# Kernel tuning notes

Measured on AMD Instinct MI355X. Metric: run time of the kernel, lower is better.

Reference implementation:

```python
import jax, jax.numpy as jnp
import numpy as np

D_IN, D_OUT, K = 128, 128, 64
X_MIN, X_MAX = 0.0, 1.0
EPS = 1e-12


def _pchip_slopes(y, x):
    # y: [..., K], x: [K] strictly increasing -> slopes [..., K]. Assumes K >= 3.
    h = x[1:] - x[:-1]                      # [K-1]
    delta = (y[..., 1:] - y[..., :-1]) / (h + EPS)
    h0, h1 = h[:-1], h[1:]
    w1 = 2.0 * h1 + h0
    w2 = h1 + 2.0 * h0
    d0_, d1_ = delta[..., :-1], delta[..., 1:]
    same_sign = d0_ * d1_ > 0
    denom = w1 / (d0_ + EPS) + w2 / (d1_ + EPS)
    d_int = jnp.where(same_sign, (w1 + w2) / (denom + EPS), 0.0)  # [..., K-2]
    d_first = ((2.0 * h[0] + h[1]) * delta[..., 0] - h[0] * delta[..., 1]) / (h[0] + h[1] + EPS)
    d_last = ((2.0 * h[-1] + h[-2]) * delta[..., -1] - h[-1] * delta[..., -2]) / (h[-1] + h[-2] + EPS)

    def limit(di, de):
        di = jnp.where(di * de <= 0, 0.0, di)
        return jnp.where(jnp.abs(di) > 3.0 * jnp.abs(de), 3.0 * de, di)

    d_first = limit(d_first, delta[..., 0])
    d_last = limit(d_last, delta[..., -1])
    return jnp.concatenate([d_first[..., None], d_int, d_last[..., None]], axis=-1)


def setup_inputs() -> dict:
    key = jax.random.key(0)
    k1, k2 = jax.random.split(key)
    x = jax.random.normal(k1, (4096, D_IN), dtype=jnp.float32)
    coeffs = 0.2 * jax.random.normal(k2, (D_OUT, D_IN, K), dtype=jnp.float32)
    bias = jnp.zeros((D_OUT,), dtype=jnp.float32)
    knots = jnp.linspace(X_MIN, X_MAX, K, dtype=jnp.float32)
    return {"x": x, "coeffs": coeffs, "bias": bias, "knots": knots}


def reference(x, coeffs, bias, knots):
    B = x.shape[0]
    slopes = _pchip_slopes(coeffs, knots)              # [d_out, d_in, K]
    h = (X_MAX - X_MIN) / (K - 1)

    xc = jnp.clip(x, X_MIN, X_MAX)                     # [B, d_in]
    idx = jnp.clip(jnp.floor((xc - X_MIN) / h).astype(jnp.int32), 0, K - 2)
    t = (xc - (X_MIN + idx.astype(x.dtype) * h)) / h   # [B, d_in]
    t2 = t * t
    t3 = t2 * t
    h00 = 2 * t3 - 3 * t2 + 1
    h10 = t3 - 2 * t2 + t
    h01 = -2 * t3 + 3 * t2
    h11 = t3 - t2

    ct = jnp.transpose(coeffs, (1, 2, 0))              # [d_in, K, d_out]
    dt = jnp.transpose(slopes, (1, 2, 0))              # [d_in, K, d_out]
    ii = jnp.arange(D_IN)[None, :]                     # [1, d_in]
    y0 = ct[ii, idx]                                   # [B, d_in, d_out]
    y1 = ct[ii, idx + 1]
    d0 = dt[ii, idx]
    d1 = dt[ii, idx + 1]

    yi = (h00[..., None] * y0 + h10[..., None] * h * d0
          + h01[..., None] * y1 + h11[..., None] * h * d1)  # [B, d_in, d_out]

    # linear extrapolation beyond the knot range
    y_left = ct[:, 0, :][None] + dt[:, 0, :][None] * (x - X_MIN)[..., None]
    y_right = ct[:, -1, :][None] + dt[:, -1, :][None] * (x - X_MAX)[..., None]
    yi = jnp.where((x < X_MIN)[..., None], y_left, yi)
    yi = jnp.where((x > X_MAX)[..., None], y_right, yi)

    return yi.sum(axis=1) + bias[None, :]              # [B, d_out]
```

## Files before the change

kernel.cpp:

```cpp
#include <hip/hip_runtime.h>

#define KN 64
#define DIN 128
#define DOUT 128
#define EPSF 1e-12f
#define HF (1.0f / 63.0f)

typedef _Float16 h2 __attribute__((ext_vector_type(2)));

#if defined(__has_builtin)
#if __has_builtin(__builtin_amdgcn_fdot2)
#define FDOT2(a, b, c) __builtin_amdgcn_fdot2((a), (b), (c), false)
#endif
#endif
#ifndef FDOT2
static __device__ __forceinline__ float FDOT2(h2 a, h2 b, float c) {
    return c + (float)a.x * (float)b.x + (float)a.y * (float)b.y;
}
#endif


__global__ __launch_bounds__(256) void kan_precompute(
    const float* __restrict__ coeffs,
    const float* __restrict__ knots,
    unsigned int* __restrict__ tb)
{
    const int i      = blockIdx.x >> 1;
    const int o_base = (blockIdx.x & 1) << 6;
    const int wave   = threadIdx.x >> 6;
    const int lane   = threadIdx.x & 63;

    __shared__ float ys[64][65];
    __shared__ float ds[64][65];

    float kn  = knots[lane];
    float kn1 = (lane < 63) ? knots[lane + 1] : 0.0f;
    float hk  = kn1 - kn;
    float hm1 = __shfl_up(hk, 1);
    float h1v = __shfl_down(hk, 1);
    float hm2 = __shfl_up(hk, 2);

    for (int ol = wave; ol < 64; ol += 4) {
        const int o = o_base + ol;
        float y = coeffs[(o * DIN + i) * KN + lane];
        float ynext = __shfl_down(y, 1);
        float delta = (lane < 63) ? (ynext - y) / (hk + EPSF) : 0.0f;
        float dm1 = __shfl_up(delta, 1);

        float w1v = 2.0f * hk + hm1;
        float w2v = hk + 2.0f * hm1;
        float denom = w1v / (dm1 + EPSF) + w2v / (delta + EPSF);
        float d = (dm1 * delta > 0.0f) ? (w1v + w2v) / (denom + EPSF) : 0.0f;

        float d1v = __shfl_down(delta, 1);
        if (lane == 0) {
            float df = ((2.0f * hk + h1v) * delta - hk * d1v) / (hk + h1v + EPSF);
            if (df * delta <= 0.0f) df = 0.0f;
            else if (fabsf(df) > 3.0f * fabsf(delta)) df = 3.0f * delta;
            d = df;
        }
        float dm2 = __shfl_up(delta, 2);
        if (lane == 63) {
            float dl = ((2.0f * hm1 + hm2) * dm1 - hm1 * dm2) / (hm1 + hm2 + EPSF);
            if (dl * dm1 <= 0.0f) dl = 0.0f;
            else if (fabsf(dl) > 3.0f * fabsf(dm1)) dl = 3.0f * dm1;
            d = dl;
        }
        ys[ol][lane] = y;
        ds[ol][lane] = d * HF;
    }
    __syncthreads();

    const int ol = threadIdx.x & 63;
    const int kb = threadIdx.x >> 6;
    for (int k = kb; k < KN; k += 4) {
        h2 v;
        v.x = (_Float16)ys[ol][k];
        v.y = (_Float16)ds[ol][k];
        tb[(i * KN + k) * DOUT + o_base + ol] = __builtin_bit_cast(unsigned int, v);
    }
}

__global__ __launch_bounds__(256) void kan_main(
    const float* __restrict__ x,
    const uint2* __restrict__ tb2,
    const float* __restrict__ bias,
    float* __restrict__ out)
{
    const int b0   = blockIdx.x << 2;
    const int tid  = threadIdx.x;
    const int wv   = tid >> 6;
    const int lane = tid & 63;

    __shared__ uint4 wl[4][DIN];

    #pragma unroll
    for (int p = tid; p < 4 * DIN; p += 256) {
        const int bl = p >> 7;
        const int i  = p & 127;
        float xv = x[(b0 + bl) * DIN + i];
        float xc = fminf(fmaxf(xv, 0.0f), 1.0f);
        int idx = (int)floorf(xc * 63.0f);
        idx = idx < 0 ? 0 : (idx > 62 ? 62 : idx);
        float t = xc * 63.0f - (float)idx;
        float t2 = t * t, t3 = t2 * t;
        float w0 = 2.0f * t3 - 3.0f * t2 + 1.0f;
        float w1 = t3 - 2.0f * t2 + t;
        float w2 = 3.0f * t2 - 2.0f * t3;
        float w3 = t3 - t2;
        if (xv < 0.0f)      { w0 = 1.0f; w1 = xv * 63.0f; w2 = 0.0f; w3 = 0.0f; idx = 0; }
        else if (xv > 1.0f) { w0 = 0.0f; w1 = 0.0f; w2 = 1.0f; w3 = (xv - 1.0f) * 63.0f; idx = 62; }
        h2 w01; w01.x = (_Float16)w0; w01.y = (_Float16)w1;
        h2 w23; w23.x = (_Float16)w2; w23.y = (_Float16)w3;
        uint4 q;
        q.x = __builtin_bit_cast(unsigned int, w01);
        q.y = __builtin_bit_cast(unsigned int, w23);
        q.z = (unsigned int)idx;
        q.w = 0u;
        wl[bl][i] = q;
    }
    __syncthreads();

    float acc0 = 0.0f, acc1 = 0.0f;
    #pragma unroll 8
    for (int i = 0; i < DIN; ++i) {
        uint4 q = wl[wv][i];
        h2 w01 = __builtin_bit_cast(h2, q.x);
        h2 w23 = __builtin_bit_cast(h2, q.y);
        int base = ((i << 6) + (int)q.z) * 64 + lane;
        uint2 A = tb2[base];
        uint2 B = tb2[base + 64];
        acc0 = FDOT2(w01, __builtin_bit_cast(h2, A.x), acc0);
        acc0 = FDOT2(w23, __builtin_bit_cast(h2, B.x), acc0);
        acc1 = FDOT2(w01, __builtin_bit_cast(h2, A.y), acc1);
        acc1 = FDOT2(w23, __builtin_bit_cast(h2, B.y), acc1);
    }

    const int o0 = lane << 1;
    float2 bo = *reinterpret_cast<const float2*>(&bias[o0]);
    float2 r; r.x = acc0 + bo.x; r.y = acc1 + bo.y;
    *reinterpret_cast<float2*>(&out[(b0 + wv) * DOUT + o0]) = r;
}

extern "C" void kernel_launch(void* const* d_in, const int* in_sizes, int n_in,
                              void* d_out, int out_size, void* d_ws, size_t ws_size,
                              hipStream_t stream) {
    const float* x      = (const float*)d_in[0];
    const float* coeffs = (const float*)d_in[1];
    const float* bias   = (const float*)d_in[2];
    const float* knots  = (const float*)d_in[3];
    float* out = (float*)d_out;
    unsigned int* tb = (unsigned int*)d_ws;

    kan_precompute<<<256, 256, 0, stream>>>(coeffs, knots, tb);
    kan_main<<<1024, 256, 0, stream>>>(x, (const uint2*)tb, bias, out);
}
```

Baseline: 107.5 us.

## Store adjacent-knot pairs in table and split d_in across waves

The precompute table now stores, for each (input, segment, output), the fp16 value/slope pair for both knot k and knot k+1 together. The main kernel can then fetch all four operands with a single 16-byte load per lane instead of two 8-byte loads from separate rows. The main kernel also splits the 128 inputs across two waves per batch row and combines the partial sums through shared memory, doubling the grid to 2048 blocks. This adds a synchronisation, doubles the table's footprint, and spreads the precompute over more, smaller blocks.

```diff
diff --git a/kernel.cpp b/kernel.cpp
--- a/kernel.cpp
+++ b/kernel.cpp
@@ -23,15 +23,15 @@
 __global__ __launch_bounds__(256) void kan_precompute(
     const float* __restrict__ coeffs,
     const float* __restrict__ knots,
-    unsigned int* __restrict__ tb)
+    uint2* __restrict__ tb)
 {
-    const int i      = blockIdx.x >> 1;
-    const int o_base = (blockIdx.x & 1) << 6;
+    const int i      = blockIdx.x >> 2;
+    const int o_base = (blockIdx.x & 3) << 5;
     const int wave   = threadIdx.x >> 6;
     const int lane   = threadIdx.x & 63;
 
-    __shared__ float ys[64][65];
-    __shared__ float ds[64][65];
+    __shared__ float ys[32][65];
+    __shared__ float ds[32][65];
 
     float kn  = knots[lane];
     float kn1 = (lane < 63) ? knots[lane + 1] : 0.0f;
@@ -40,8 +40,10 @@
     float h1v = __shfl_down(hk, 1);
     float hm2 = __shfl_up(hk, 2);
 
-    for (int ol = wave; ol < 64; ol += 4) {
-        const int o = o_base + ol;
+    #pragma unroll
+    for (int m = 0; m < 8; ++m) {
+        const int ol = wave + (m << 2);
+        const int o  = o_base + ol;
         float y = coeffs[(o * DIN + i) * KN + lane];
         float ynext = __shfl_down(y, 1);
         float delta = (lane < 63) ? (ynext - y) / (hk + EPSF) : 0.0f;
@@ -71,34 +73,42 @@
     }
     __syncthreads();
 
-    const int ol = threadIdx.x & 63;
-    const int kb = threadIdx.x >> 6;
-    for (int k = kb; k < KN; k += 4) {
-        h2 v;
-        v.x = (_Float16)ys[ol][k];
-        v.y = (_Float16)ds[ol][k];
-        tb[(i * KN + k) * DOUT + o_base + ol] = __builtin_bit_cast(unsigned int, v);
+    const int ol2 = threadIdx.x & 31;
+    const int j0  = threadIdx.x >> 5;
+    #pragma unroll
+    for (int m = 0; m < 8; ++m) {
+        const int j = j0 + (m << 3);
+        if (j < 63) {
+            h2 lo; lo.x = (_Float16)ys[ol2][j];     lo.y = (_Float16)ds[ol2][j];
+            h2 hi; hi.x = (_Float16)ys[ol2][j + 1]; hi.y = (_Float16)ds[ol2][j + 1];
+            uint2 v;
+            v.x = __builtin_bit_cast(unsigned int, lo);
+            v.y = __builtin_bit_cast(unsigned int, hi);
+            tb[((i << 6) + j) * DOUT + o_base + ol2] = v;
+        }
     }
 }
 
 __global__ __launch_bounds__(256) void kan_main(
     const float* __restrict__ x,
-    const uint2* __restrict__ tb2,
+    const uint4* __restrict__ tb4,
     const float* __restrict__ bias,
     float* __restrict__ out)
 {
-    const int b0   = blockIdx.x << 2;
+    const int b0   = blockIdx.x << 1;
     const int tid  = threadIdx.x;
     const int wv   = tid >> 6;
+    const int bl   = wv >> 1;
+    const int half = wv & 1;
     const int lane = tid & 63;
 
-    __shared__ uint4 wl[4][DIN];
+    __shared__ uint4  wl[2][DIN];
+    __shared__ float2 red[2][64];
 
-    #pragma unroll
-    for (int p = tid; p < 4 * DIN; p += 256) {
-        const int bl = p >> 7;
-        const int i  = p & 127;
-        float xv = x[(b0 + bl) * DIN + i];
+    {
+        const int bl1 = tid >> 7;
+        const int i1  = tid & 127;
+        float xv = x[(b0 + bl1) * DIN + i1];
         float xc = fminf(fmaxf(xv, 0.0f), 1.0f);
         int idx = (int)floorf(xc * 63.0f);
         idx = idx < 0 ? 0 : (idx > 62 ? 62 : idx);
@@ -117,29 +127,37 @@
         q.y = __builtin_bit_cast(unsigned int, w23);
         q.z = (unsigned int)idx;
         q.w = 0u;
-        wl[bl][i] = q;
+        wl[bl1][i1] = q;
     }
     __syncthreads();
 
     float acc0 = 0.0f, acc1 = 0.0f;
+    const int ibase = half << 6;
     #pragma unroll 8
-    for (int i = 0; i < DIN; ++i) {
-        uint4 q = wl[wv][i];
+    for (int ii = 0; ii < 64; ++ii) {
+        const int i = ibase + ii;
+        uint4 q = wl[bl][i];
         h2 w01 = __builtin_bit_cast(h2, q.x);
         h2 w23 = __builtin_bit_cast(h2, q.y);
-        int base = ((i << 6) + (int)q.z) * 64 + lane;
-        uint2 A = tb2[base];
-        uint2 B = tb2[base + 64];
-        acc0 = FDOT2(w01, __builtin_bit_cast(h2, A.x), acc0);
-        acc0 = FDOT2(w23, __builtin_bit_cast(h2, B.x), acc0);
-        acc1 = FDOT2(w01, __builtin_bit_cast(h2, A.y), acc1);
-        acc1 = FDOT2(w23, __builtin_bit_cast(h2, B.y), acc1);
+        unsigned off = (((unsigned)(i << 6) + q.z) << 6) + (unsigned)lane;
+        uint4 r = tb4[off];
+        acc0 = FDOT2(w01, __builtin_bit_cast(h2, r.x), acc0);
+        acc0 = FDOT2(w23, __builtin_bit_cast(h2, r.y), acc0);
+        acc1 = FDOT2(w01, __builtin_bit_cast(h2, r.z), acc1);
+        acc1 = FDOT2(w23, __builtin_bit_cast(h2, r.w), acc1);
     }
 
-    const int o0 = lane << 1;
-    float2 bo = *reinterpret_cast<const float2*>(&bias[o0]);
-    float2 r; r.x = acc0 + bo.x; r.y = acc1 + bo.y;
-    *reinterpret_cast<float2*>(&out[(b0 + wv) * DOUT + o0]) = r;
+    if (half) red[bl][lane] = make_float2(acc0, acc1);
+    __syncthreads();
+    if (!half) {
+        float2 r2 = red[bl][lane];
+        const int o0 = lane << 1;
+        float2 bo = *reinterpret_cast<const float2*>(&bias[o0]);
+        float2 res;
+        res.x = acc0 + r2.x + bo.x;
+        res.y = acc1 + r2.y + bo.y;
+        *reinterpret_cast<float2*>(&out[(b0 + bl) * DOUT + o0]) = res;
+    }
 }
 
 extern "C" void kernel_launch(void* const* d_in, const int* in_sizes, int n_in,
@@ -150,8 +168,8 @@
     const float* bias   = (const float*)d_in[2];
     const float* knots  = (const float*)d_in[3];
     float* out = (float*)d_out;
-    unsigned int* tb = (unsigned int*)d_ws;
+    uint2* tb = (uint2*)d_ws;
 
-    kan_precompute<<<256, 256, 0, stream>>>(coeffs, knots, tb);
-    kan_main<<<1024, 256, 0, stream>>>(x, (const uint2*)tb, bias, out);
+    kan_precompute<<<512, 256, 0, stream>>>(coeffs, knots, tb);
+    kan_main<<<2048, 256, 0, stream>>>(x, (const uint4*)tb, bias, out);
 }
```

Result: faster. 93.78 us (-12.8%).

## Split extrapolated inputs into single-load list and split input dim across waves

Applied to the files above, without the earlier changes.

Each wave now handles half of the input features for one batch row, sorting them via ballot into extrapolated (one table row needed) and interior (two rows) lists in LDS. Extrapolated features do one load and two dot products instead of two loads and four, skipping the zero-weighted half. The two half-waves' partial sums are combined through shared memory, and the grid doubles to keep the same total work. Since x is standard normal, about 2/3 of features fall outside [0,1], so fewer gather loads are issued, at the cost of an extra reduction, a barrier and data-dependent loop trip counts.

```diff
diff --git a/kernel.cpp b/kernel.cpp
--- a/kernel.cpp
+++ b/kernel.cpp
@@ -87,59 +87,90 @@
     const float* __restrict__ bias,
     float* __restrict__ out)
 {
-    const int b0   = blockIdx.x << 2;
-    const int tid  = threadIdx.x;
-    const int wv   = tid >> 6;
-    const int lane = tid & 63;
+    const int b0    = blockIdx.x << 1;
+    const int tid   = threadIdx.x;
+    const int wv    = tid >> 6;
+    const int lane  = tid & 63;
+    const int bl    = wv >> 1;
+    const int ihalf = wv & 1;
 
-    __shared__ uint4 wl[4][DIN];
+    __shared__ uint4  listI[4][64];
+    __shared__ uint2  listE[4][64];
+    __shared__ float2 red[2][64];
 
-    #pragma unroll
-    for (int p = tid; p < 4 * DIN; p += 256) {
-        const int bl = p >> 7;
-        const int i  = p & 127;
-        float xv = x[(b0 + bl) * DIN + i];
-        float xc = fminf(fmaxf(xv, 0.0f), 1.0f);
-        int idx = (int)floorf(xc * 63.0f);
-        idx = idx < 0 ? 0 : (idx > 62 ? 62 : idx);
-        float t = xc * 63.0f - (float)idx;
+    const int i = (ihalf << 6) + lane;
+    float xv = x[(b0 + bl) * DIN + i];
+    const bool ext = (xv < 0.0f) || (xv > 1.0f);
+    unsigned long long mE = __ballot(ext);
+    const int nE = __popcll(mE);
+    const int nI = 64 - nE;
+    const unsigned long long below = (1ULL << lane) - 1ULL;
+
+    if (ext) {
+        int slot = __popcll(mE & below);
+        float tt = (xv < 0.0f) ? xv * 63.0f : (xv - 1.0f) * 63.0f;
+        int k = (xv < 0.0f) ? 0 : 63;
+        h2 w01; w01.x = (_Float16)1.0f; w01.y = (_Float16)tt;
+        uint2 e;
+        e.x = __builtin_bit_cast(unsigned int, w01);
+        e.y = (unsigned)(((i << 6) + k) << 6);
+        listE[wv][slot] = e;
+    } else {
+        int slot = __popcll((~mE) & below);
+        int idx = (int)(xv * 63.0f);
+        idx = idx > 62 ? 62 : idx;
+        float t = xv * 63.0f - (float)idx;
         float t2 = t * t, t3 = t2 * t;
         float w0 = 2.0f * t3 - 3.0f * t2 + 1.0f;
         float w1 = t3 - 2.0f * t2 + t;
         float w2 = 3.0f * t2 - 2.0f * t3;
         float w3 = t3 - t2;
-        if (xv < 0.0f)      { w0 = 1.0f; w1 = xv * 63.0f; w2 = 0.0f; w3 = 0.0f; idx = 0; }
-        else if (xv > 1.0f) { w0 = 0.0f; w1 = 0.0f; w2 = 1.0f; w3 = (xv - 1.0f) * 63.0f; idx = 62; }
         h2 w01; w01.x = (_Float16)w0; w01.y = (_Float16)w1;
         h2 w23; w23.x = (_Float16)w2; w23.y = (_Float16)w3;
         uint4 q;
         q.x = __builtin_bit_cast(unsigned int, w01);
         q.y = __builtin_bit_cast(unsigned int, w23);
-        q.z = (unsigned int)idx;
+        q.z = (unsigned)(((i << 6) + idx) << 6);
         q.w = 0u;
-        wl[bl][i] = q;
+        listI[wv][slot] = q;
     }
-    __syncthreads();
 
     float acc0 = 0.0f, acc1 = 0.0f;
-    #pragma unroll 8
-    for (int i = 0; i < DIN; ++i) {
-        uint4 q = wl[wv][i];
+    const uint2* tp = tb2 + lane;
+
+    #pragma unroll 4
+    for (int n = 0; n < nE; ++n) {
+        uint2 e = listE[wv][n];
+        h2 w01 = __builtin_bit_cast(h2, e.x);
+        uint2 r = tp[e.y];
+        acc0 = FDOT2(w01, __builtin_bit_cast(h2, r.x), acc0);
+        acc1 = FDOT2(w01, __builtin_bit_cast(h2, r.y), acc1);
+    }
+
+    #pragma unroll 4
+    for (int n = 0; n < nI; ++n) {
+        uint4 q = listI[wv][n];
         h2 w01 = __builtin_bit_cast(h2, q.x);
         h2 w23 = __builtin_bit_cast(h2, q.y);
-        int base = ((i << 6) + (int)q.z) * 64 + lane;
-        uint2 A = tb2[base];
-        uint2 B = tb2[base + 64];
-        acc0 = FDOT2(w01, __builtin_bit_cast(h2, A.x), acc0);
-        acc0 = FDOT2(w23, __builtin_bit_cast(h2, B.x), acc0);
-        acc1 = FDOT2(w01, __builtin_bit_cast(h2, A.y), acc1);
-        acc1 = FDOT2(w23, __builtin_bit_cast(h2, B.y), acc1);
+        uint2 rA = tp[q.z];
+        uint2 rB = tp[q.z + 64];
+        acc0 = FDOT2(w01, __builtin_bit_cast(h2, rA.x), acc0);
+        acc0 = FDOT2(w23, __builtin_bit_cast(h2, rB.x), acc0);
+        acc1 = FDOT2(w01, __builtin_bit_cast(h2, rA.y), acc1);
+        acc1 = FDOT2(w23, __builtin_bit_cast(h2, rB.y), acc1);
     }
 
-    const int o0 = lane << 1;
-    float2 bo = *reinterpret_cast<const float2*>(&bias[o0]);
-    float2 r; r.x = acc0 + bo.x; r.y = acc1 + bo.y;
-    *reinterpret_cast<float2*>(&out[(b0 + wv) * DOUT + o0]) = r;
+    if (ihalf) red[bl][lane] = make_float2(acc0, acc1);
+    __syncthreads();
+    if (!ihalf) {
+        float2 r2 = red[bl][lane];
+        const int o0 = lane << 1;
+        float2 bo = *reinterpret_cast<const float2*>(&bias[o0]);
+        float2 res;
+        res.x = acc0 + r2.x + bo.x;
+        res.y = acc1 + r2.y + bo.y;
+        *reinterpret_cast<float2*>(&out[(b0 + bl) * DOUT + o0]) = res;
+    }
 }
 
 extern "C" void kernel_launch(void* const* d_in, const int* in_sizes, int n_in,
@@ -153,5 +184,5 @@
     unsigned int* tb = (unsigned int*)d_ws;
 
     kan_precompute<<<256, 256, 0, stream>>>(coeffs, knots, tb);
-    kan_main<<<1024, 256, 0, stream>>>(x, (const uint2*)tb, bias, out);
+    kan_main<<<2048, 256, 0, stream>>>(x, (const uint2*)tb, bias, out);
 }
```

Measured after the change: 99.14 us. -7.8%, faster.

## Split input-dimension loop across two waves per batch row with LDS reduction

Applied to the files above, without the earlier changes.

Each block now handles 2 batch rows instead of 4, with two waves per row each covering half of the 128 input features. The partial sums are combined through shared memory before the bias add and store. The precomputed table offset is also folded into the LDS entry to trim per-iteration index arithmetic. This shortens each wave's serial gather chain and doubles the grid to expose more parallelism, at the cost of an extra barrier, an LDS reduction and twice as many blocks each recomputing weights.

```diff
diff --git a/kernel.cpp b/kernel.cpp
--- a/kernel.cpp
+++ b/kernel.cpp
@@ -87,18 +87,20 @@
     const float* __restrict__ bias,
     float* __restrict__ out)
 {
-    const int b0   = blockIdx.x << 2;
+    const int b0   = blockIdx.x << 1;
     const int tid  = threadIdx.x;
     const int wv   = tid >> 6;
+    const int bl   = wv >> 1;
+    const int half = wv & 1;
     const int lane = tid & 63;
 
-    __shared__ uint4 wl[4][DIN];
+    __shared__ uint4  wl[2][DIN];
+    __shared__ float2 red[2][64];
 
-    #pragma unroll
-    for (int p = tid; p < 4 * DIN; p += 256) {
-        const int bl = p >> 7;
-        const int i  = p & 127;
-        float xv = x[(b0 + bl) * DIN + i];
+    {
+        const int bl1 = tid >> 7;
+        const int i1  = tid & 127;
+        float xv = x[(b0 + bl1) * DIN + i1];
         float xc = fminf(fmaxf(xv, 0.0f), 1.0f);
         int idx = (int)floorf(xc * 63.0f);
         idx = idx < 0 ? 0 : (idx > 62 ? 62 : idx);
@@ -115,31 +117,40 @@
         uint4 q;
         q.x = __builtin_bit_cast(unsigned int, w01);
         q.y = __builtin_bit_cast(unsigned int, w23);
-        q.z = (unsigned int)idx;
+        q.z = (unsigned)(((i1 << 6) + idx) << 6);
         q.w = 0u;
-        wl[bl][i] = q;
+        wl[bl1][i1] = q;
     }
     __syncthreads();
 
     float acc0 = 0.0f, acc1 = 0.0f;
+    const int ibase = half << 6;
+    const uint2* tp = tb2 + lane;
+
     #pragma unroll 8
-    for (int i = 0; i < DIN; ++i) {
-        uint4 q = wl[wv][i];
+    for (int ii = 0; ii < 64; ++ii) {
+        uint4 q = wl[bl][ibase + ii];
         h2 w01 = __builtin_bit_cast(h2, q.x);
         h2 w23 = __builtin_bit_cast(h2, q.y);
-        int base = ((i << 6) + (int)q.z) * 64 + lane;
-        uint2 A = tb2[base];
-        uint2 B = tb2[base + 64];
-        acc0 = FDOT2(w01, __builtin_bit_cast(h2, A.x), acc0);
-        acc0 = FDOT2(w23, __builtin_bit_cast(h2, B.x), acc0);
-        acc1 = FDOT2(w01, __builtin_bit_cast(h2, A.y), acc1);
-        acc1 = FDOT2(w23, __builtin_bit_cast(h2, B.y), acc1);
+        uint2 rA = tp[q.z];
+        uint2 rB = tp[q.z + 64];
+        acc0 = FDOT2(w01, __builtin_bit_cast(h2, rA.x), acc0);
+        acc0 = FDOT2(w23, __builtin_bit_cast(h2, rB.x), acc0);
+        acc1 = FDOT2(w01, __builtin_bit_cast(h2, rA.y), acc1);
+        acc1 = FDOT2(w23, __builtin_bit_cast(h2, rB.y), acc1);
     }
 
-    const int o0 = lane << 1;
-    float2 bo = *reinterpret_cast<const float2*>(&bias[o0]);
-    float2 r; r.x = acc0 + bo.x; r.y = acc1 + bo.y;
-    *reinterpret_cast<float2*>(&out[(b0 + wv) * DOUT + o0]) = r;
+    if (half) red[bl][lane] = make_float2(acc0, acc1);
+    __syncthreads();
+    if (!half) {
+        float2 r2 = red[bl][lane];
+        const int o0 = lane << 1;
+        float2 bo = *reinterpret_cast<const float2*>(&bias[o0]);
+        float2 res;
+        res.x = acc0 + r2.x + bo.x;
+        res.y = acc1 + r2.y + bo.y;
+        *reinterpret_cast<float2*>(&out[(b0 + bl) * DOUT + o0]) = res;
+    }
 }
 
 extern "C" void kernel_launch(void* const* d_in, const int* in_sizes, int n_in,
@@ -153,5 +164,5 @@
     unsigned int* tb = (unsigned int*)d_ws;
 
     kan_precompute<<<256, 256, 0, stream>>>(coeffs, knots, tb);
-    kan_main<<<1024, 256, 0, stream>>>(x, (const uint2*)tb, bias, out);
+    kan_main<<<2048, 256, 0, stream>>>(x, (const uint2*)tb, bias, out);
 }
```

Result: no change. 107.6 us (+0.1%).
